# Optimization experiments

Hardware: AMD Instinct MI355X
Metric: run time of the kernel (lower is better)

Reference implementation:

```python
import jax, jax.numpy as jnp
import numpy as np

T, B, I, H, L = 1024, 16, 1024, 1024, 2


def setup_inputs() -> dict:
    key = jax.random.key(0)
    ks = jax.random.split(key, 1 + 4 * L)
    k = 1.0 / np.sqrt(H)
    inp = {"x": jax.random.normal(ks[0], (T, B, I), dtype=jnp.float32)}
    for l in range(L):
        base = 1 + 4 * l
        in_dim = I if l == 0 else H
        inp[f"Wih_{l}"] = jax.random.uniform(ks[base + 0], (4 * H, in_dim), minval=-k, maxval=k, dtype=jnp.float32)
        inp[f"bih_{l}"] = jax.random.uniform(ks[base + 1], (4 * H,), minval=-k, maxval=k, dtype=jnp.float32)
        inp[f"Whh_{l}"] = jax.random.uniform(ks[base + 2], (4 * H, H), minval=-k, maxval=k, dtype=jnp.float32)
        inp[f"bhh_{l}"] = jax.random.uniform(ks[base + 3], (4 * H,), minval=-k, maxval=k, dtype=jnp.float32)
    return inp


def _lstm_layer(x, Wih, bih, Whh, bhh):
    # x: [T, B, in_dim] time-major. Returns (outputs [T,B,H], h_T [B,H], c_T [B,H]).
    Hd = Whh.shape[1]
    Bn = x.shape[1]
    h0 = jnp.zeros((Bn, Hd), dtype=x.dtype)
    c0 = jnp.zeros((Bn, Hd), dtype=x.dtype)
    # Precompute input projection for all timesteps in one big GEMM.
    gx = jnp.einsum('tbi,gi->tbg', x, Wih) + bih  # [T, B, 4H]

    def step(carry, gxt):
        h, c = carry
        gates = gxt + h @ Whh.T + bhh  # [B, 4H]
        i, f, g, o = jnp.split(gates, 4, axis=1)
        i = jax.nn.sigmoid(i)
        f = jax.nn.sigmoid(f)
        g = jnp.tanh(g)
        o = jax.nn.sigmoid(o)
        c = f * c + i * g
        h = o * jnp.tanh(c)
        return (h, c), h

    (hT, cT), ys = jax.lax.scan(step, (h0, c0), gx)
    return ys, hT, cT


def reference(x, Wih_0, bih_0, Whh_0, bhh_0, Wih_1, bih_1, Whh_1, bhh_1):
    out0, h0, c0 = _lstm_layer(x, Wih_0, bih_0, Whh_0, bhh_0)
    out1, h1, c1 = _lstm_layer(out0, Wih_1, bih_1, Whh_1, bhh_1)
    next_h = jnp.stack([h0, h1])  # [num_layers, B, H]
    next_c = jnp.stack([c0, c1])
    return out1, (next_h, next_c)
```

## Files before the change

### kernel.cpp

```cpp
#include <hip/hip_runtime.h>


#define T_STEPS 1024
#define TQ 16

typedef unsigned short u16;
typedef unsigned long long u64;
typedef __attribute__((ext_vector_type(8))) __bf16 bf16x8;
typedef __attribute__((ext_vector_type(4))) float float4v;
typedef __attribute__((ext_vector_type(4))) unsigned short ushort4v;
typedef __attribute__((ext_vector_type(8))) unsigned short ushort8;

__device__ __forceinline__ float bf2f(u16 h) {
    unsigned u = ((unsigned)h) << 16;
    return __builtin_bit_cast(float, u);
}
__device__ __forceinline__ u16 f2bf(float f) {
    unsigned u = __builtin_bit_cast(unsigned, f);
    u += 0x7fff + ((u >> 16) & 1);
    return (u16)(u >> 16);
}

__device__ __forceinline__ float4v mfma16(bf16x8 a, bf16x8 b, float4v c) {
    return __builtin_amdgcn_mfma_f32_16x16x32_bf16(a, b, c, 0, 0, 0);
}
__device__ __forceinline__ unsigned aload(const unsigned* p) {
    return __hip_atomic_load(p, __ATOMIC_RELAXED, __HIP_MEMORY_SCOPE_AGENT);
}
__device__ __forceinline__ void astore(unsigned* p, unsigned v) {
    __hip_atomic_store(p, v, __ATOMIC_RELAXED, __HIP_MEMORY_SCOPE_AGENT);
}
__device__ __forceinline__ void gld_lds16c(const void* g, void* l) {
    __builtin_amdgcn_global_load_lds(
        (const __attribute__((address_space(1))) unsigned*)g,
        (__attribute__((address_space(3))) unsigned*)l, 16, 0, 0);
}
__device__ __forceinline__ void gld_lds16b(const void* g, void* l) {
    __builtin_amdgcn_global_load_lds(
        (const __attribute__((address_space(1))) unsigned*)g,
        (__attribute__((address_space(3))) unsigned*)l, 16, 0, 17);
}

__global__ void init_zero(unsigned* __restrict__ flags0,
                          unsigned* __restrict__ flags1,
                          unsigned* __restrict__ h0,
                          unsigned* __restrict__ h1) {
    int i = blockIdx.x * 256 + threadIdx.x;
    const int N0 = 65600, N1 = 256, N2 = 8192, N3 = 8192;
    for (int k = i; k < N0 + N1 + N2 + N3; k += 64 * 256) {
        if (k < N0) flags0[k] = 0u;
        else if (k < N0 + N1) flags1[k - N0] = 0u;
        else if (k < N0 + N1 + N2) h0[k - N0 - N1] = 0u;
        else h1[k - N0 - N1 - N2] = 0u;
    }
}

__device__ __forceinline__ void pack_one(const float* src, u16* dst, int tile, int rowbase) {
    int tid = threadIdx.x;
    ushort8* d = (ushort8*)dst;
#pragma unroll
    for (int it = 0; it < 8; ++it) {
        int c = tid + it * 256;
        int kc = c >> 6, lane = c & 63;
        const float4v* s4 = (const float4v*)(src + (((long)(rowbase + (lane & 15))) << 10)
                                                 + (kc << 5) + ((lane >> 4) << 3));
        float4v lo = s4[0], hi = s4[1];
        ushort8 o;
        o[0] = f2bf(lo[0]); o[1] = f2bf(lo[1]); o[2] = f2bf(lo[2]); o[3] = f2bf(lo[3]);
        o[4] = f2bf(hi[0]); o[5] = f2bf(hi[1]); o[6] = f2bf(hi[2]); o[7] = f2bf(hi[3]);
        d[tile * 2048 + c] = o;
    }
}

__global__ void pack_x(const float* __restrict__ src, u16* __restrict__ dst) {
    pack_one(src, dst, blockIdx.x, blockIdx.x << 4);
}

__global__ void pack_w(const float* __restrict__ w0, const float* __restrict__ w1,
                       const float* __restrict__ w2, const float* __restrict__ w3,
                       u16* __restrict__ d0, u16* __restrict__ d1,
                       u16* __restrict__ d2, u16* __restrict__ d3) {
    int which = blockIdx.x >> 8, tile = blockIdx.x & 255;
    const float* s = (which == 0) ? w0 : (which == 1) ? w1 : (which == 2) ? w2 : w3;
    u16* d = (which == 0) ? d0 : (which == 1) ? d1 : (which == 2) ? d2 : d3;
    int rowbase = ((tile & 3) << 10) + ((tile >> 2) << 4);
    pack_one(s, d, tile, rowbase);
}

__global__ __launch_bounds__(256, 1) void gx_gemm(
        const u16* __restrict__ xp, const bf16x8* __restrict__ wp,
        const float* __restrict__ bih, const float* __restrict__ bhh,
        u16* __restrict__ gx) {
    __shared__ u64 abuf[4096];
    __shared__ float4v part[4][4][64];
    int blk = blockIdx.x, tq = blockIdx.y;
    int tid = threadIdx.x, w = tid >> 6, L = tid & 63;
    int gc = (w << 10) + (blk << 4) + (L & 15);
    float bsum = bih[gc] + bhh[gc];

    bf16x8 wf[32];
#pragma unroll
    for (int g = 0; g < 4; ++g) {
        const bf16x8* wpt = wp + (blk * 4 + g) * 2048 + (w * 8) * 64 + L;
#pragma unroll
        for (int k = 0; k < 8; ++k) wf[g * 8 + k] = wpt[k * 64];
    }
    const bf16x8* hp = (const bf16x8*)abuf;

    const int tch = T_STEPS / TQ;
    for (int tt = 0; tt < tch; ++tt) {
        int t = tq * tch + tt;
        const char* src = (const char*)xp + ((size_t)t << 15) + (w << 13) + (L << 4);
        char* dst = (char*)abuf + (w << 13);
#pragma unroll
        for (int i = 0; i < 8; ++i) gld_lds16c(src + i * 1024, dst + i * 1024);
        __builtin_amdgcn_s_waitcnt(0);
        __builtin_amdgcn_sched_barrier(0);

        float4v acc[4];
#pragma unroll
        for (int g = 0; g < 4; ++g) acc[g] = float4v{0.f, 0.f, 0.f, 0.f};
#pragma unroll
        for (int k = 0; k < 8; ++k) {
            bf16x8 a = hp[(8 * w + k) * 64 + L];
#pragma unroll
            for (int g = 0; g < 4; ++g) acc[g] = mfma16(a, wf[g * 8 + k], acc[g]);
        }
#pragma unroll
        for (int g = 0; g < 4; ++g) part[w][g][L] = acc[g];
        __syncthreads();
        float4v s = part[0][w][L] + part[1][w][L] + part[2][w][L] + part[3][w][L];
        ushort4v o;
#pragma unroll
        for (int r = 0; r < 4; ++r) o[r] = f2bf(s[r] + bsum);
        ((ushort4v*)gx)[((t * 64 + blk) * 4 + w) * 64 + L] = o;
        __syncthreads();
    }
}

__global__ __launch_bounds__(256, 1) void lstm_scan2(
        const u16* __restrict__ gx0,
        const bf16x8* __restrict__ wpHh0,
        const bf16x8* __restrict__ wpIh1, const bf16x8* __restrict__ wpHh1,
        const float* __restrict__ bih1, const float* __restrict__ bhh1,
        unsigned* hist0w,
        unsigned* hist1x,
        unsigned* h1s0,
        unsigned* flags0,
        unsigned* flags1,
        float* outbase) {
    __shared__ u64 hbufA[4096];
    __shared__ u64 hbufB[4096];
    __shared__ float4v lds_part[4][4][64];
    __shared__ float4v lds_g[4][64];

    int tid = threadIdx.x, w = tid >> 6, L = tid & 63;
    int m = tid >> 4, j = tid & 15;
    int Lc = ((m >> 2) << 4) | j, rr = m & 3;
    int layer = (blockIdx.x >= 64);
    int blk = blockIdx.x & 63;
    int hcol = (blk << 4) + j;
    int kcw = hcol >> 5, laneg = (hcol >> 3) & 3, jj = hcol & 7;
    int hwoff32 = ((kcw * 64 + m + (laneg << 4)) << 2) + (jj >> 1);
    float* fH = outbase + 16777216 + (layer ? 16384 : 0);
    float* fC = outbase + 16777216 + 32768 + (layer ? 16384 : 0);
    float c = 0.f;

    if (!layer) {
        bf16x8 wf[32];
#pragma unroll
        for (int g = 0; g < 4; ++g) {
            const bf16x8* wpt = wpHh0 + (blk * 4 + g) * 2048 + (w * 8) * 64 + L;
#pragma unroll
            for (int k = 0; k < 8; ++k) wf[g * 8 + k] = wpt[k * 64];
        }
        const bf16x8* hp = (const bf16x8*)hbufA;

        for (int t = 0; t < T_STEPS; ++t) {
            ushort4v gxv = ((const ushort4v*)gx0)[((t * 64 + blk) * 4 + w) * 64 + L];
            if (t > 0) {
                unsigned v;
                do { v = aload(&flags0[t * 64 + L]); }
                while (__ballot(v != 0u) != ~0ull);
            }
            {
                const char* src = (const char*)hist0w + ((size_t)t << 15) + (w << 13) + (L << 4);
                char* dst = (char*)hbufA + (w << 13);
#pragma unroll
                for (int i = 0; i < 8; ++i) gld_lds16b(src + i * 1024, dst + i * 1024);
            }
            __builtin_amdgcn_s_waitcnt(0);
            __builtin_amdgcn_sched_barrier(0);

            float4v acc[4];
#pragma unroll
            for (int g = 0; g < 4; ++g) acc[g] = float4v{0.f, 0.f, 0.f, 0.f};
#pragma unroll
            for (int k = 0; k < 8; ++k) {
                bf16x8 a = hp[(8 * w + k) * 64 + L];
#pragma unroll
                for (int g = 0; g < 4; ++g) acc[g] = mfma16(a, wf[g * 8 + k], acc[g]);
            }
#pragma unroll
            for (int g = 0; g < 4; ++g) lds_part[w][g][L] = acc[g];
            __syncthreads();

            float4v s = lds_part[0][w][L] + lds_part[1][w][L]
                      + lds_part[2][w][L] + lds_part[3][w][L];
            float4v g4;
#pragma unroll
            for (int r = 0; r < 4; ++r) g4[r] = s[r] + bf2f(gxv[r]);
            lds_g[w][L] = g4;
            __syncthreads();

            float gi = lds_g[0][Lc][rr], gf = lds_g[1][Lc][rr];
            float gg = lds_g[2][Lc][rr], go = lds_g[3][Lc][rr];
            float iv = 1.f / (1.f + __expf(-gi));
            float fv = 1.f / (1.f + __expf(-gf));
            float gv = 1.f - 2.f / (1.f + __expf(2.f * gg));
            float ov = 1.f / (1.f + __expf(-go));
            c = fv * c + iv * gv;
            float h = ov * (1.f - 2.f / (1.f + __expf(2.f * c)));
            unsigned hb = f2bf(h);

            unsigned other = (unsigned)__shfl_xor((int)hb, 1);
            if (!(tid & 1))
                astore(hist0w + ((size_t)(t + 1) << 13) + hwoff32, hb | (other << 16));
            if (t == T_STEPS - 1) {
                fH[(m << 10) + hcol] = h;
                fC[(m << 10) + hcol] = c;
            }
            __builtin_amdgcn_s_waitcnt(0);
            __syncthreads();
            if (tid == 0) astore(&flags0[(t + 1) * 64 + blk], 1u);
        }
    } else {
        bf16x8 wi[32], wh[32];
#pragma unroll
        for (int g = 0; g < 4; ++g) {
            const bf16x8* p1 = wpIh1 + (blk * 4 + g) * 2048 + (w * 8) * 64 + L;
            const bf16x8* p2 = wpHh1 + (blk * 4 + g) * 2048 + (w * 8) * 64 + L;
#pragma unroll
            for (int k = 0; k < 8; ++k) { wi[g * 8 + k] = p1[k * 64]; wh[g * 8 + k] = p2[k * 64]; }
        }
        int gc = (w << 10) + (blk << 4) + (L & 15);
        float bsum = bih1[gc] + bhh1[gc];
        const bf16x8* hA = (const bf16x8*)hbufA;
        const bf16x8* hB = (const bf16x8*)hbufB;

        for (int t = 0; t < T_STEPS; ++t) {
            {
                unsigned v0, v1;
                do {
                    v0 = aload(&flags0[(t + 1) * 64 + L]);
                    v1 = (t > 0) ? aload(&flags1[(t & 3) * 64 + L]) : (unsigned)t;
                } while (__ballot(v0 != 0u && v1 == (unsigned)t) != ~0ull);
            }
            {
                const char* sa = (const char*)hist0w + ((size_t)(t + 1) << 15) + (w << 13) + (L << 4);
                const char* sb = (t == 0)
                    ? ((const char*)h1s0 + (w << 13) + (L << 4))
                    : ((const char*)hist1x + ((size_t)(t - 1) << 15) + (w << 13) + (L << 4));
                char* da = (char*)hbufA + (w << 13);
                char* db = (char*)hbufB + (w << 13);
#pragma unroll
                for (int i = 0; i < 8; ++i) gld_lds16b(sa + i * 1024, da + i * 1024);
#pragma unroll
                for (int i = 0; i < 8; ++i) gld_lds16b(sb + i * 1024, db + i * 1024);
            }
            __builtin_amdgcn_s_waitcnt(0);
            __builtin_amdgcn_sched_barrier(0);

            float4v acc[4];
#pragma unroll
            for (int g = 0; g < 4; ++g) acc[g] = float4v{0.f, 0.f, 0.f, 0.f};
#pragma unroll
            for (int k = 0; k < 8; ++k) {
                bf16x8 a = hA[(8 * w + k) * 64 + L];
                bf16x8 b = hB[(8 * w + k) * 64 + L];
#pragma unroll
                for (int g = 0; g < 4; ++g) acc[g] = mfma16(a, wi[g * 8 + k], acc[g]);
#pragma unroll
                for (int g = 0; g < 4; ++g) acc[g] = mfma16(b, wh[g * 8 + k], acc[g]);
            }
#pragma unroll
            for (int g = 0; g < 4; ++g) lds_part[w][g][L] = acc[g];
            __syncthreads();

            float4v s = lds_part[0][w][L] + lds_part[1][w][L]
                      + lds_part[2][w][L] + lds_part[3][w][L];
            float4v g4;
#pragma unroll
            for (int r = 0; r < 4; ++r) g4[r] = s[r] + bsum;
            lds_g[w][L] = g4;
            __syncthreads();

            float gi = lds_g[0][Lc][rr], gf = lds_g[1][Lc][rr];
            float gg = lds_g[2][Lc][rr], go = lds_g[3][Lc][rr];
            float iv = 1.f / (1.f + __expf(-gi));
            float fv = 1.f / (1.f + __expf(-gf));
            float gv = 1.f - 2.f / (1.f + __expf(2.f * gg));
            float ov = 1.f / (1.f + __expf(-go));
            c = fv * c + iv * gv;
            float h = ov * (1.f - 2.f / (1.f + __expf(2.f * c)));
            unsigned hb = f2bf(h);

            unsigned other = (unsigned)__shfl_xor((int)hb, 1);
            if (!(tid & 1))
                astore(hist1x + ((size_t)t << 13) + hwoff32, hb | (other << 16));
            outbase[(t << 14) + (m << 10) + hcol] = h;
            if (t == T_STEPS - 1) {
                fH[(m << 10) + hcol] = h;
                fC[(m << 10) + hcol] = c;
            }
            __builtin_amdgcn_s_waitcnt(0);
            __syncthreads();
            if (tid == 0) astore(&flags1[(((t + 1) & 3) << 6) + blk], (unsigned)(t + 1));
        }
    }
}

extern "C" void kernel_launch(void* const* d_in, const int* in_sizes, int n_in,
                              void* d_out, int out_size, void* d_ws, size_t ws_size,
                              hipStream_t stream) {
    const float* x    = (const float*)d_in[0];
    const float* Wih0 = (const float*)d_in[1];
    const float* bih0 = (const float*)d_in[2];
    const float* Whh0 = (const float*)d_in[3];
    const float* bhh0 = (const float*)d_in[4];
    const float* Wih1 = (const float*)d_in[5];
    const float* bih1 = (const float*)d_in[6];
    const float* Whh1 = (const float*)d_in[7];
    const float* bhh1 = (const float*)d_in[8];
    float* out = (float*)d_out;

    char* ws = (char*)d_ws;
    u16* wpIh0 = (u16*)(ws + 0);
    u16* wpHh0 = (u16*)(ws + 8388608);
    u16* wpIh1 = (u16*)(ws + 16777216);
    u16* wpHh1 = (u16*)(ws + 25165824);
    u16* xpack = (u16*)(ws + 33554432);
    u16* hist0 = (u16*)(ws + 67108864);
    u16* h1s0  = (u16*)(ws + 100696064);
    u16* gxbuf = (u16*)(ws + 100728832);
    unsigned* flags0 = (unsigned*)(ws + 234946560);
    unsigned* flags1 = (unsigned*)(ws + 235208960);

    init_zero<<<dim3(64), dim3(256), 0, stream>>>(flags0, flags1,
                                                  (unsigned*)hist0, (unsigned*)h1s0);
    pack_w<<<dim3(1024), dim3(256), 0, stream>>>(Wih0, Whh0, Wih1, Whh1,
                                                 wpIh0, wpHh0, wpIh1, wpHh1);
    pack_x<<<dim3(1024), dim3(256), 0, stream>>>(x, xpack);
    gx_gemm<<<dim3(64, TQ), dim3(256), 0, stream>>>(
        xpack, (const bf16x8*)wpIh0, bih0, bhh0, gxbuf);
    lstm_scan2<<<dim3(128), dim3(256), 0, stream>>>(
        gxbuf, (const bf16x8*)wpHh0, (const bf16x8*)wpIh1, (const bf16x8*)wpHh1,
        bih1, bhh1, (unsigned*)hist0, (unsigned*)xpack, (unsigned*)h1s0,
        flags0, flags1, out);
}
```

Baseline: 5.432 ms.

## Double waves per block in LSTM scan, splitting K reduction across eight waves

```diff
diff --git a/kernel.cpp b/kernel.cpp
--- a/kernel.cpp
+++ b/kernel.cpp
@@ -138,7 +138,7 @@
     }
 }
 
-__global__ __launch_bounds__(256, 1) void lstm_scan2(
+__global__ __launch_bounds__(512, 1) void lstm_scan2(
         const u16* __restrict__ gx0,
         const bf16x8* __restrict__ wpHh0,
         const bf16x8* __restrict__ wpIh1, const bf16x8* __restrict__ wpHh1,
@@ -149,9 +149,8 @@
         unsigned* flags0,
         unsigned* flags1,
         float* outbase) {
-    __shared__ u64 hbufA[4096];
-    __shared__ u64 hbufB[4096];
-    __shared__ float4v lds_part[4][4][64];
+    __shared__ u64 hbuf[8192];
+    __shared__ float4v lds_part[8][4][64];
     __shared__ float4v lds_g[4][64];
 
     int tid = threadIdx.x, w = tid >> 6, L = tid & 63;
@@ -165,29 +164,30 @@
     float* fH = outbase + 16777216 + (layer ? 16384 : 0);
     float* fC = outbase + 16777216 + 32768 + (layer ? 16384 : 0);
     float c = 0.f;
+    const bf16x8* hp = (const bf16x8*)hbuf;
 
     if (!layer) {
-        bf16x8 wf[32];
+        bf16x8 wf[16];
 #pragma unroll
         for (int g = 0; g < 4; ++g) {
-            const bf16x8* wpt = wpHh0 + (blk * 4 + g) * 2048 + (w * 8) * 64 + L;
-#pragma unroll
-            for (int k = 0; k < 8; ++k) wf[g * 8 + k] = wpt[k * 64];
-        }
-        const bf16x8* hp = (const bf16x8*)hbufA;
+            const bf16x8* wsrc = wpHh0 + (blk * 4 + g) * 2048 + (4 * w) * 64 + L;
+#pragma unroll
+            for (int k = 0; k < 4; ++k) wf[g * 4 + k] = wsrc[k * 64];
+        }
 
         for (int t = 0; t < T_STEPS; ++t) {
-            ushort4v gxv = ((const ushort4v*)gx0)[((t * 64 + blk) * 4 + w) * 64 + L];
+            ushort4v gxv = {0, 0, 0, 0};
+            if (w < 4) gxv = ((const ushort4v*)gx0)[((t * 64 + blk) * 4 + w) * 64 + L];
             if (t > 0) {
                 unsigned v;
                 do { v = aload(&flags0[t * 64 + L]); }
                 while (__ballot(v != 0u) != ~0ull);
             }
             {
-                const char* src = (const char*)hist0w + ((size_t)t << 15) + (w << 13) + (L << 4);
-                char* dst = (char*)hbufA + (w << 13);
-#pragma unroll
-                for (int i = 0; i < 8; ++i) gld_lds16b(src + i * 1024, dst + i * 1024);
+                const char* src = (const char*)hist0w + ((size_t)t << 15) + (w << 12) + (L << 4);
+                char* dst = (char*)hbuf + (w << 12);
+#pragma unroll
+                for (int i = 0; i < 4; ++i) gld_lds16b(src + i * 1024, dst + i * 1024);
             }
             __builtin_amdgcn_s_waitcnt(0);
             __builtin_amdgcn_sched_barrier(0);
@@ -196,6 +196,89 @@
 #pragma unroll
             for (int g = 0; g < 4; ++g) acc[g] = float4v{0.f, 0.f, 0.f, 0.f};
 #pragma unroll
+            for (int k = 0; k < 4; ++k) {
+                bf16x8 a = hp[(4 * w + k) * 64 + L];
+#pragma unroll
+                for (int g = 0; g < 4; ++g) acc[g] = mfma16(a, wf[g * 4 + k], acc[g]);
+            }
+#pragma unroll
+            for (int g = 0; g < 4; ++g) lds_part[w][g][L] = acc[g];
+            __syncthreads();
+
+            if (w < 4) {
+                float4v s = lds_part[0][w][L] + lds_part[1][w][L]
+                          + lds_part[2][w][L] + lds_part[3][w][L]
+                          + lds_part[4][w][L] + lds_part[5][w][L]
+                          + lds_part[6][w][L] + lds_part[7][w][L];
+                float4v g4;
+#pragma unroll
+                for (int r = 0; r < 4; ++r) g4[r] = s[r] + bf2f(gxv[r]);
+                lds_g[w][L] = g4;
+            }
+            __syncthreads();
+
+            if (tid < 256) {
+                float gi = lds_g[0][Lc][rr], gf = lds_g[1][Lc][rr];
+                float gg = lds_g[2][Lc][rr], go = lds_g[3][Lc][rr];
+                float iv = 1.f / (1.f + __expf(-gi));
+                float fv = 1.f / (1.f + __expf(-gf));
+                float gv = 1.f - 2.f / (1.f + __expf(2.f * gg));
+                float ov = 1.f / (1.f + __expf(-go));
+                c = fv * c + iv * gv;
+                float h = ov * (1.f - 2.f / (1.f + __expf(2.f * c)));
+                unsigned hb = f2bf(h);
+                unsigned other = (unsigned)__shfl_xor((int)hb, 1);
+                if (!(tid & 1))
+                    astore(hist0w + ((size_t)(t + 1) << 13) + hwoff32, hb | (other << 16));
+                if (t == T_STEPS - 1) {
+                    fH[(m << 10) + hcol] = h;
+                    fC[(m << 10) + hcol] = c;
+                }
+            }
+            __builtin_amdgcn_s_waitcnt(0);
+            __syncthreads();
+            if (tid == 0) astore(&flags0[(t + 1) * 64 + blk], 1u);
+        }
+    } else {
+        bf16x8 wf[32];
+#pragma unroll
+        for (int g = 0; g < 4; ++g) {
+            const bf16x8* wsrc = (w < 4)
+                ? (wpIh1 + (blk * 4 + g) * 2048 + (8 * w) * 64 + L)
+                : (wpHh1 + (blk * 4 + g) * 2048 + (8 * (w - 4)) * 64 + L);
+#pragma unroll
+            for (int k = 0; k < 8; ++k) wf[g * 8 + k] = wsrc[k * 64];
+        }
+        int gc = (w << 10) + (blk << 4) + (L & 15);
+        float bsum = (w < 4) ? (bih1[gc] + bhh1[gc]) : 0.f;
+
+        for (int t = 0; t < T_STEPS; ++t) {
+            if (w < 4) {
+                unsigned v;
+                do { v = aload(&flags0[(t + 1) * 64 + L]); }
+                while (__ballot(v != 0u) != ~0ull);
+            } else if (t > 0) {
+                unsigned v;
+                do { v = aload(&flags1[(t & 3) * 64 + L]); }
+                while (__ballot(v == (unsigned)t) != ~0ull);
+            }
+            {
+                const char* src = (w < 4)
+                    ? ((const char*)hist0w + ((size_t)(t + 1) << 15) + (w << 13) + (L << 4))
+                    : ((t == 0)
+                        ? ((const char*)h1s0 + ((w - 4) << 13) + (L << 4))
+                        : ((const char*)hist1x + ((size_t)(t - 1) << 15) + ((w - 4) << 13) + (L << 4)));
+                char* dst = (char*)hbuf + (w << 13);
+#pragma unroll
+                for (int i = 0; i < 8; ++i) gld_lds16b(src + i * 1024, dst + i * 1024);
+            }
+            __builtin_amdgcn_s_waitcnt(0);
+            __builtin_amdgcn_sched_barrier(0);
+
+            float4v acc[4];
+#pragma unroll
+            for (int g = 0; g < 4; ++g) acc[g] = float4v{0.f, 0.f, 0.f, 0.f};
+#pragma unroll
             for (int k = 0; k < 8; ++k) {
                 bf16x8 a = hp[(8 * w + k) * 64 + L];
 #pragma unroll
@@ -205,117 +288,43 @@
             for (int g = 0; g < 4; ++g) lds_part[w][g][L] = acc[g];
             __syncthreads();
 
-            float4v s = lds_part[0][w][L] + lds_part[1][w][L]
-                      + lds_part[2][w][L] + lds_part[3][w][L];
-            float4v g4;
-#pragma unroll
-            for (int r = 0; r < 4; ++r) g4[r] = s[r] + bf2f(gxv[r]);
-            lds_g[w][L] = g4;
-            __syncthreads();
-
-            float gi = lds_g[0][Lc][rr], gf = lds_g[1][Lc][rr];
-            float gg = lds_g[2][Lc][rr], go = lds_g[3][Lc][rr];
-            float iv = 1.f / (1.f + __expf(-gi));
-            float fv = 1.f / (1.f + __expf(-gf));
-            float gv = 1.f - 2.f / (1.f + __expf(2.f * gg));
-            float ov = 1.f / (1.f + __expf(-go));
-            c = fv * c + iv * gv;
-            float h = ov * (1.f - 2.f / (1.f + __expf(2.f * c)));
-            unsigned hb = f2bf(h);
-
-            unsigned other = (unsigned)__shfl_xor((int)hb, 1);
-            if (!(tid & 1))
-                astore(hist0w + ((size_t)(t + 1) << 13) + hwoff32, hb | (other << 16));
-            if (t == T_STEPS - 1) {
-                fH[(m << 10) + hcol] = h;
-                fC[(m << 10) + hcol] = c;
+            if (w < 4) {
+                float4v s = lds_part[0][w][L] + lds_part[1][w][L]
+                          + lds_part[2][w][L] + lds_part[3][w][L]
+                          + lds_part[4][w][L] + lds_part[5][w][L]
+                          + lds_part[6][w][L] + lds_part[7][w][L];
+                float4v g4;
+#pragma unroll
+                for (int r = 0; r < 4; ++r) g4[r] = s[r] + bsum;
+                lds_g[w][L] = g4;
+            }
+            __syncthreads();
+
+            float h = 0.f;
+            if (tid < 256) {
+                float gi = lds_g[0][Lc][rr], gf = lds_g[1][Lc][rr];
+                float gg = lds_g[2][Lc][rr], go = lds_g[3][Lc][rr];
+                float iv = 1.f / (1.f + __expf(-gi));
+                float fv = 1.f / (1.f + __expf(-gf));
+                float gv = 1.f - 2.f / (1.f + __expf(2.f * gg));
+                float ov = 1.f / (1.f + __expf(-go));
+                c = fv * c + iv * gv;
+                h = ov * (1.f - 2.f / (1.f + __expf(2.f * c)));
+                unsigned hb = f2bf(h);
+                unsigned other = (unsigned)__shfl_xor((int)hb, 1);
+                if (!(tid & 1))
+                    astore(hist1x + ((size_t)t << 13) + hwoff32, hb | (other << 16));
             }
             __builtin_amdgcn_s_waitcnt(0);
             __syncthreads();
-            if (tid == 0) astore(&flags0[(t + 1) * 64 + blk], 1u);
-        }
-    } else {
-        bf16x8 wi[32], wh[32];
-#pragma unroll
-        for (int g = 0; g < 4; ++g) {
-            const bf16x8* p1 = wpIh1 + (blk * 4 + g) * 2048 + (w * 8) * 64 + L;
-            const bf16x8* p2 = wpHh1 + (blk * 4 + g) * 2048 + (w * 8) * 64 + L;
-#pragma unroll
-            for (int k = 0; k < 8; ++k) { wi[g * 8 + k] = p1[k * 64]; wh[g * 8 + k] = p2[k * 64]; }
-        }
-        int gc = (w << 10) + (blk << 4) + (L & 15);
-        float bsum = bih1[gc] + bhh1[gc];
-        const bf16x8* hA = (const bf16x8*)hbufA;
-        const bf16x8* hB = (const bf16x8*)hbufB;
-
-        for (int t = 0; t < T_STEPS; ++t) {
-            {
-                unsigned v0, v1;
-                do {
-                    v0 = aload(&flags0[(t + 1) * 64 + L]);
-                    v1 = (t > 0) ? aload(&flags1[(t & 3) * 64 + L]) : (unsigned)t;
-                } while (__ballot(v0 != 0u && v1 == (unsigned)t) != ~0ull);
-            }
-            {
-                const char* sa = (const char*)hist0w + ((size_t)(t + 1) << 15) + (w << 13) + (L << 4);
-                const char* sb = (t == 0)
-                    ? ((const char*)h1s0 + (w << 13) + (L << 4))
-                    : ((const char*)hist1x + ((size_t)(t - 1) << 15) + (w << 13) + (L << 4));
-                char* da = (char*)hbufA + (w << 13);
-                char* db = (char*)hbufB + (w << 13);
-#pragma unroll
-                for (int i = 0; i < 8; ++i) gld_lds16b(sa + i * 1024, da + i * 1024);
-#pragma unroll
-                for (int i = 0; i < 8; ++i) gld_lds16b(sb + i * 1024, db + i * 1024);
-            }
-            __builtin_amdgcn_s_waitcnt(0);
-            __builtin_amdgcn_sched_barrier(0);
-
-            float4v acc[4];
-#pragma unroll
-            for (int g = 0; g < 4; ++g) acc[g] = float4v{0.f, 0.f, 0.f, 0.f};
-#pragma unroll
-            for (int k = 0; k < 8; ++k) {
-                bf16x8 a = hA[(8 * w + k) * 64 + L];
-                bf16x8 b = hB[(8 * w + k) * 64 + L];
-#pragma unroll
-                for (int g = 0; g < 4; ++g) acc[g] = mfma16(a, wi[g * 8 + k], acc[g]);
-#pragma unroll
-                for (int g = 0; g < 4; ++g) acc[g] = mfma16(b, wh[g * 8 + k], acc[g]);
-            }
-#pragma unroll
-            for (int g = 0; g < 4; ++g) lds_part[w][g][L] = acc[g];
-            __syncthreads();
-
-            float4v s = lds_part[0][w][L] + lds_part[1][w][L]
-                      + lds_part[2][w][L] + lds_part[3][w][L];
-            float4v g4;
-#pragma unroll
-            for (int r = 0; r < 4; ++r) g4[r] = s[r] + bsum;
-            lds_g[w][L] = g4;
-            __syncthreads();
-
-            float gi = lds_g[0][Lc][rr], gf = lds_g[1][Lc][rr];
-            float gg = lds_g[2][Lc][rr], go = lds_g[3][Lc][rr];
-            float iv = 1.f / (1.f + __expf(-gi));
-            float fv = 1.f / (1.f + __expf(-gf));
-            float gv = 1.f - 2.f / (1.f + __expf(2.f * gg));
-            float ov = 1.f / (1.f + __expf(-go));
-            c = fv * c + iv * gv;
-            float h = ov * (1.f - 2.f / (1.f + __expf(2.f * c)));
-            unsigned hb = f2bf(h);
-
-            unsigned other = (unsigned)__shfl_xor((int)hb, 1);
-            if (!(tid & 1))
-                astore(hist1x + ((size_t)t << 13) + hwoff32, hb | (other << 16));
-            outbase[(t << 14) + (m << 10) + hcol] = h;
-            if (t == T_STEPS - 1) {
-                fH[(m << 10) + hcol] = h;
-                fC[(m << 10) + hcol] = c;
-            }
-            __builtin_amdgcn_s_waitcnt(0);
-            __syncthreads();
             if (tid == 0) astore(&flags1[(((t + 1) & 3) << 6) + blk], (unsigned)(t + 1));
+            if (tid < 256) {
+                outbase[(t << 14) + (m << 10) + hcol] = h;
+                if (t == T_STEPS - 1) {
+                    fH[(m << 10) + hcol] = h;
+                    fC[(m << 10) + hcol] = c;
+                }
+            }
         }
     }
 }
@@ -353,7 +362,7 @@
     pack_x<<<dim3(1024), dim3(256), 0, stream>>>(x, xpack);
     gx_gemm<<<dim3(64, TQ), dim3(256), 0, stream>>>(
         xpack, (const bf16x8*)wpIh0, bih0, bhh0, gxbuf);
-    lstm_scan2<<<dim3(128), dim3(256), 0, stream>>>(
+    lstm_scan2<<<dim3(128), dim3(512), 0, stream>>>(
         gxbuf, (const bf16x8*)wpHh0, (const bf16x8*)wpIh1, (const bf16x8*)wpHh1,
         bih1, bhh1, (unsigned*)hist0, (unsigned*)xpack, (unsigned*)h1s0,
         flags0, flags1, out);
```

After: 5.003 ms. 7.9% less time.
